# Performance work log

Hardware: AMD Instinct MI355X
Metric: run time of the kernel (lower is better)

The kernel has to match this reference:

```python
import jax, jax.numpy as jnp
import numpy as np
import math

D = 768
H = 12
HD = D // H  # 64
DFF = 4 * D


def _layernorm(x, g, b, eps=1e-5):
    mu = jnp.mean(x, axis=-1, keepdims=True)
    var = jnp.var(x, axis=-1, keepdims=True)
    return (x - mu) * jax.lax.rsqrt(var + eps) * g + b


def _new_gelu(x):
    c = math.sqrt(2.0 / math.pi)
    return 0.5 * x * (1.0 + jnp.tanh(c * (x + 0.044715 * x * x * x)))


def setup_inputs() -> dict:
    key = jax.random.key(0)
    ks = jax.random.split(key, 8)
    B, N = 8, 1024
    s = 0.02
    return {
        "x": jax.random.normal(ks[0], (B, N, D), jnp.float32),
        "pad_mask": jnp.ones((B, N), jnp.int32),
        "ln1_g": jnp.ones((D,), jnp.float32),
        "ln1_b": jnp.zeros((D,), jnp.float32),
        "w_attn": jax.random.normal(ks[1], (D, 3 * D), jnp.float32) * s,
        "b_attn": jnp.zeros((3 * D,), jnp.float32),
        "w_proj": jax.random.normal(ks[2], (D, D), jnp.float32) * s,
        "b_proj": jnp.zeros((D,), jnp.float32),
        "ln2_g": jnp.ones((D,), jnp.float32),
        "ln2_b": jnp.zeros((D,), jnp.float32),
        "w_fc": jax.random.normal(ks[3], (D, DFF), jnp.float32) * s,
        "b_fc": jnp.zeros((DFF,), jnp.float32),
        "w_fc2": jax.random.normal(ks[4], (DFF, D), jnp.float32) * s,
        "b_fc2": jnp.zeros((D,), jnp.float32),
    }


def reference(x, pad_mask, ln1_g, ln1_b, w_attn, b_attn, w_proj, b_proj,
              ln2_g, ln2_b, w_fc, b_fc, w_fc2, b_fc2):
    B, N, C = x.shape
    # --- attention branch (note: source's causal masked_fill is NOT in-place,
    # so the causal mask is effectively never applied; only pad_mask is) ---
    h = _layernorm(x, ln1_g, ln1_b)
    qkv = h @ w_attn + b_attn  # [B,N,3D]
    q, k, v = jnp.split(qkv, 3, axis=-1)
    q = q.reshape(B, N, H, HD).transpose(0, 2, 1, 3)  # [B,H,N,hd]
    k = k.reshape(B, N, H, HD).transpose(0, 2, 1, 3)
    v = v.reshape(B, N, H, HD).transpose(0, 2, 1, 3)
    att = jnp.einsum('bhqd,bhkd->bhqk', q, k) * (1.0 / math.sqrt(HD))
    # pad mask broadcasts as [B,1,N,1]: masks query rows where pad==0
    att = jnp.where(pad_mask[:, None, :, None] == 0, -jnp.inf, att)
    att = jax.nn.softmax(att, axis=-1)
    o = jnp.einsum('bhqk,bhkd->bhqd', att, v)
    o = o.transpose(0, 2, 1, 3).reshape(B, N, C)
    x = x + (o @ w_proj + b_proj)
    # --- MLP branch ---
    h2 = _layernorm(x, ln2_g, ln2_b)
    x = x + (_new_gelu(h2 @ w_fc + b_fc) @ w_fc2 + b_fc2)
    return x
```

## Files before the change

### kernel.cpp

```cpp
#include <hip/hip_runtime.h>
#include <hip/hip_bf16.h>

typedef __bf16 bf16;
typedef __bf16 bf16x8 __attribute__((ext_vector_type(8)));
typedef __bf16 bf16x4 __attribute__((ext_vector_type(4)));
typedef float f32x4 __attribute__((ext_vector_type(4)));

#define SEQ 1024
#define BATCH 8
#define DM 768
#define NH 12
#define HDIM 64
#define DFF 3072
#define NTOK (BATCH*SEQ)

#define AS1 __attribute__((address_space(1)))
#define AS3 __attribute__((address_space(3)))
#define MFMA16(a, b, c) __builtin_amdgcn_mfma_f32_16x16x32_bf16(a, b, c, 0, 0, 0)

__device__ __forceinline__ float gelu_f(float x) {
  const float c = 0.7978845608028654f;
  float z = c * (x + 0.044715f * x * x * x);
  return x / (1.0f + __expf(-2.0f * z));
}

__global__ __launch_bounds__(256) void transpose4_kernel(
    const float* __restrict__ in0, bf16* __restrict__ out0,
    const float* __restrict__ in1, bf16* __restrict__ out1,
    const float* __restrict__ in2, bf16* __restrict__ out2,
    const float* __restrict__ in3, bf16* __restrict__ out3) {
  __shared__ float tile[32][33];
  int id = blockIdx.x;
  const float* in; bf16* out; int R, C;
  if (id < 1728)      { in = in0; out = out0; R = 768;  C = 2304; }
  else if (id < 2304) { in = in1; out = out1; R = 768;  C = 768;  id -= 1728; }
  else if (id < 4608) { in = in2; out = out2; R = 768;  C = 3072; id -= 2304; }
  else                { in = in3; out = out3; R = 3072; C = 768;  id -= 4608; }
  int nc = C >> 5;
  int c0 = (id % nc) * 32, r0 = (id / nc) * 32;
  int tx = threadIdx.x & 31, ty = threadIdx.x >> 5;
  #pragma unroll
  for (int i = 0; i < 4; ++i)
    tile[ty + i * 8][tx] = in[(size_t)(r0 + ty + i * 8) * C + c0 + tx];
  __syncthreads();
  #pragma unroll
  for (int i = 0; i < 4; ++i)
    out[(size_t)(c0 + ty + i * 8) * R + r0 + tx] = (bf16)tile[tx][ty + i * 8];
}

__global__ __launch_bounds__(256) void ln_kernel(
    const float* __restrict__ x, const float* __restrict__ g,
    const float* __restrict__ bta, bf16* __restrict__ out) {
  int row = blockIdx.x;
  int tid = threadIdx.x;
  const float* xr = x + (size_t)row * DM;
  float v0 = xr[tid], v1 = xr[tid + 256], v2 = xr[tid + 512];
  float s1 = v0 + v1 + v2;
  float s2 = v0 * v0 + v1 * v1 + v2 * v2;
  #pragma unroll
  for (int m = 32; m >= 1; m >>= 1) {
    s1 += __shfl_xor(s1, m, 64);
    s2 += __shfl_xor(s2, m, 64);
  }
  __shared__ float ps1[4], ps2[4];
  int wid = tid >> 6;
  if ((tid & 63) == 0) { ps1[wid] = s1; ps2[wid] = s2; }
  __syncthreads();
  float t1 = ps1[0] + ps1[1] + ps1[2] + ps1[3];
  float t2 = ps2[0] + ps2[1] + ps2[2] + ps2[3];
  float mean = t1 * (1.0f / DM);
  float var = t2 * (1.0f / DM) - mean * mean;
  float rstd = rsqrtf(var + 1e-5f);
  bf16* orow = out + (size_t)row * DM;
  orow[tid]       = (bf16)((v0 - mean) * rstd * g[tid]       + bta[tid]);
  orow[tid + 256] = (bf16)((v1 - mean) * rstd * g[tid + 256] + bta[tid + 256]);
  orow[tid + 512] = (bf16)((v2 - mean) * rstd * g[tid + 512] + bta[tid + 512]);
}

__global__ __launch_bounds__(256) void reduce_ln_kernel(
    const float* __restrict__ p0, const float* __restrict__ p1,
    const float* __restrict__ bias, const float* __restrict__ resid,
    const float* __restrict__ g, const float* __restrict__ bta,
    bf16* __restrict__ x1b, bf16* __restrict__ h) {
  int row = blockIdx.x;
  int tid = threadIdx.x;
  size_t base = (size_t)row * DM;
  float v0 = p0[base + tid]       + p1[base + tid]       + bias[tid]       + resid[base + tid];
  float v1 = p0[base + tid + 256] + p1[base + tid + 256] + bias[tid + 256] + resid[base + tid + 256];
  float v2 = p0[base + tid + 512] + p1[base + tid + 512] + bias[tid + 512] + resid[base + tid + 512];
  bf16* xr = x1b + base;
  xr[tid]       = (bf16)v0;
  xr[tid + 256] = (bf16)v1;
  xr[tid + 512] = (bf16)v2;
  float s1 = v0 + v1 + v2;
  float s2 = v0 * v0 + v1 * v1 + v2 * v2;
  #pragma unroll
  for (int m = 32; m >= 1; m >>= 1) {
    s1 += __shfl_xor(s1, m, 64);
    s2 += __shfl_xor(s2, m, 64);
  }
  __shared__ float ps1[4], ps2[4];
  int wid = tid >> 6;
  if ((tid & 63) == 0) { ps1[wid] = s1; ps2[wid] = s2; }
  __syncthreads();
  float t1 = ps1[0] + ps1[1] + ps1[2] + ps1[3];
  float t2 = ps2[0] + ps2[1] + ps2[2] + ps2[3];
  float mean = t1 * (1.0f / DM);
  float var = t2 * (1.0f / DM) - mean * mean;
  float rstd = rsqrtf(var + 1e-5f);
  bf16* orow = h + base;
  orow[tid]       = (bf16)((v0 - mean) * rstd * g[tid]       + bta[tid]);
  orow[tid + 256] = (bf16)((v1 - mean) * rstd * g[tid + 256] + bta[tid + 256]);
  orow[tid + 512] = (bf16)((v2 - mean) * rstd * g[tid + 512] + bta[tid + 512]);
}

__global__ __launch_bounds__(256) void reduce_out_kernel(
    const float* __restrict__ p0, const float* __restrict__ p1,
    const float* __restrict__ bias, const bf16* __restrict__ resid,
    float* __restrict__ out) {
  int i = blockIdx.x * 256 + threadIdx.x;
  size_t e = (size_t)i * 4;
  f32x4 a = *(const f32x4*)(p0 + e);
  f32x4 b = *(const f32x4*)(p1 + e);
  f32x4 bs = *(const f32x4*)(bias + (int)(e % DM));
  bf16x4 r = *(const bf16x4*)(resid + e);
  f32x4 o;
  #pragma unroll
  for (int j = 0; j < 4; ++j) o[j] = a[j] + b[j] + bs[j] + (float)r[j];
  *(f32x4*)(out + e) = o;
}

__global__ __launch_bounds__(512, 4) void gemm_kernel(
    const bf16* __restrict__ A, int lda, const bf16* __restrict__ BT,
    const float* __restrict__ bias, const float* __restrict__ residF,
    const bf16* __restrict__ residB,
    float* __restrict__ outF, bf16* __restrict__ outB,
    int N, int K, int flags) {
  __shared__ bf16 As[3][128 * 32];
  __shared__ bf16 Bs[3][256 * 32];
  int tid = threadIdx.x;
  int wid = tid >> 6, lane = tid & 63;
  int nct = N >> 8;
  int nwg = gridDim.x;
  int bid = blockIdx.x;
  int lid = ((nwg & 7) == 0) ? ((bid & 7) * (nwg >> 3) + (bid >> 3)) : bid;
  int row0, col0, koff = 0, Keff = K;
  size_t outOff = 0;
  if (flags & 2) {
    int half = nwg >> 1;
    int s = lid / half;
    int r = lid - s * half;
    int nrt = half / nct;
    col0 = (r / nrt) << 8;
    row0 = (r % nrt) << 7;
    Keff = K >> 1;
    koff = s * Keff;
    outOff = (size_t)s * ((size_t)nrt << 7) * (size_t)N;
  } else {
    row0 = (lid / nct) * 128;
    col0 = (lid % nct) * 256;
  }
  int wm = wid >> 2, wn = wid & 3;
  int fr = lane & 15, fq = lane >> 4;
  f32x4 acc[4][4] = {};

  int srow = tid >> 2;
  int ssl = ((tid & 3) ^ ((tid >> 3) & 3)) * 8;
  const bf16* gA  = A + (size_t)(row0 + srow) * lda + koff + ssl;
  const bf16* gB  = BT + (size_t)(col0 + srow) * K + koff + ssl;
  const bf16* gB2 = gB + (size_t)128 * K;
  int ldsA  = (wid * 16) * 32;
  int ldsB  = (wid * 16) * 32;
  int ldsB2 = (128 + wid * 16) * 32;

  int RB0 = wn * 64 + 0 * 16 + fr, RB1 = wn * 64 + 1 * 16 + fr;
  int RB2 = wn * 64 + 2 * 16 + fr, RB3 = wn * 64 + 3 * 16 + fr;
  int RA0 = wm * 64 + 0 * 16 + fr, RA1 = wm * 64 + 1 * 16 + fr;
  int RA2 = wm * 64 + 2 * 16 + fr, RA3 = wm * 64 + 3 * 16 + fr;
  int offB0 = RB0 * 32 + (fq ^ ((RB0 >> 1) & 3)) * 8;
  int offB1 = RB1 * 32 + (fq ^ ((RB1 >> 1) & 3)) * 8;
  int offB2 = RB2 * 32 + (fq ^ ((RB2 >> 1) & 3)) * 8;
  int offB3 = RB3 * 32 + (fq ^ ((RB3 >> 1) & 3)) * 8;
  int offA0 = RA0 * 32 + (fq ^ ((RA0 >> 1) & 3)) * 8;
  int offA1 = RA1 * 32 + (fq ^ ((RA1 >> 1) & 3)) * 8;
  int offA2 = RA2 * 32 + (fq ^ ((RA2 >> 1) & 3)) * 8;
  int offA3 = RA3 * 32 + (fq ^ ((RA3 >> 1) & 3)) * 8;

  int nt = Keff >> 5;

  __builtin_amdgcn_global_load_lds((const AS1 void*)(gA), (AS3 void*)(&As[0][ldsA]), 16, 0, 0);
  __builtin_amdgcn_global_load_lds((const AS1 void*)(gB), (AS3 void*)(&Bs[0][ldsB]), 16, 0, 0);
  __builtin_amdgcn_global_load_lds((const AS1 void*)(gB2), (AS3 void*)(&Bs[0][ldsB2]), 16, 0, 0);
  __builtin_amdgcn_global_load_lds((const AS1 void*)(gA + 32), (AS3 void*)(&As[1][ldsA]), 16, 0, 0);
  __builtin_amdgcn_global_load_lds((const AS1 void*)(gB + 32), (AS3 void*)(&Bs[1][ldsB]), 16, 0, 0);
  __builtin_amdgcn_global_load_lds((const AS1 void*)(gB2 + 32), (AS3 void*)(&Bs[1][ldsB2]), 16, 0, 0);

#define KS(CB, T)                                                              \
  {                                                                            \
    if ((T) == nt - 1) asm volatile("s_waitcnt vmcnt(0)" ::: "memory");        \
    else               asm volatile("s_waitcnt vmcnt(3)" ::: "memory");        \
    __builtin_amdgcn_s_barrier();                                              \
    bf16x8 b0 = *(const bf16x8*)&Bs[CB][offB0];                                \
    bf16x8 b1 = *(const bf16x8*)&Bs[CB][offB1];                                \
    bf16x8 b2 = *(const bf16x8*)&Bs[CB][offB2];                                \
    bf16x8 b3 = *(const bf16x8*)&Bs[CB][offB3];                                \
    bf16x8 a0 = *(const bf16x8*)&As[CB][offA0];                                \
    bf16x8 a1 = *(const bf16x8*)&As[CB][offA1];                                \
    if ((T) + 2 < nt)                                                          \
      __builtin_amdgcn_global_load_lds(                                        \
          (const AS1 void*)(gA + ((T) + 2) * 32),                              \
          (AS3 void*)(&As[((CB) + 2) % 3][ldsA]), 16, 0, 0);                   \
    __builtin_amdgcn_s_setprio(1);                                             \
    acc[0][0] = MFMA16(a0, b0, acc[0][0]); acc[0][1] = MFMA16(a0, b1, acc[0][1]); \
    acc[0][2] = MFMA16(a0, b2, acc[0][2]); acc[0][3] = MFMA16(a0, b3, acc[0][3]); \
    acc[1][0] = MFMA16(a1, b0, acc[1][0]); acc[1][1] = MFMA16(a1, b1, acc[1][1]); \
    acc[1][2] = MFMA16(a1, b2, acc[1][2]); acc[1][3] = MFMA16(a1, b3, acc[1][3]); \
    __builtin_amdgcn_s_setprio(0);                                             \
    bf16x8 a2 = *(const bf16x8*)&As[CB][offA2];                                \
    bf16x8 a3 = *(const bf16x8*)&As[CB][offA3];                                \
    if ((T) + 2 < nt) {                                                        \
      __builtin_amdgcn_global_load_lds(                                        \
          (const AS1 void*)(gB + ((T) + 2) * 32),                              \
          (AS3 void*)(&Bs[((CB) + 2) % 3][ldsB]), 16, 0, 0);                   \
      __builtin_amdgcn_global_load_lds(                                        \
          (const AS1 void*)(gB2 + ((T) + 2) * 32),                             \
          (AS3 void*)(&Bs[((CB) + 2) % 3][ldsB2]), 16, 0, 0);                  \
    }                                                                          \
    __builtin_amdgcn_s_setprio(1);                                             \
    acc[2][0] = MFMA16(a2, b0, acc[2][0]); acc[2][1] = MFMA16(a2, b1, acc[2][1]); \
    acc[2][2] = MFMA16(a2, b2, acc[2][2]); acc[2][3] = MFMA16(a2, b3, acc[2][3]); \
    acc[3][0] = MFMA16(a3, b0, acc[3][0]); acc[3][1] = MFMA16(a3, b1, acc[3][1]); \
    acc[3][2] = MFMA16(a3, b2, acc[3][2]); acc[3][3] = MFMA16(a3, b3, acc[3][3]); \
    __builtin_amdgcn_s_setprio(0);                                             \
  }

  for (int t = 0; t < nt; t += 3) {
    KS(0, t);
    KS(1, t + 1);
    KS(2, t + 2);
  }
#undef KS

  bool gelu = (flags & 1);
  bool qkvm = (flags & 4);
  bf16* vtp = (bf16*)outF;
  #pragma unroll
  for (int m = 0; m < 4; ++m) {
    #pragma unroll
    for (int n = 0; n < 4; ++n) {
      int col = col0 + wn * 64 + n * 16 + fr;
      float bs = bias ? bias[col] : 0.f;
      if (qkvm && col >= 2 * DM) {
        int rb = row0 + wm * 64 + m * 16 + fq * 4;
        int hcol = col - 2 * DM;
        int bh = (rb >> 10) * NH + (hcol >> 6);
        bf16x4 vv;
        #pragma unroll
        for (int r = 0; r < 4; ++r) vv[r] = (bf16)(acc[m][n][r] + bs);
        *(bf16x4*)(vtp + ((size_t)bh * HDIM + (hcol & 63)) * SEQ + (rb & 1023)) = vv;
      } else {
        #pragma unroll
        for (int r = 0; r < 4; ++r) {
          int row = row0 + wm * 64 + m * 16 + fq * 4 + r;
          float v = acc[m][n][r] + bs;
          if (gelu) v = gelu_f(v);
          if (residF) v += residF[(size_t)row * N + col];
          if (residB) v += (float)residB[(size_t)row * N + col];
          if (qkvm)        outB[(size_t)row * N + col] = (bf16)v;
          else if (outF)   outF[outOff + (size_t)row * N + col] = v;
          else             outB[(size_t)row * N + col] = (bf16)v;
        }
      }
    }
  }
}

__global__ __launch_bounds__(256) void attn_kernel(
    bf16* __restrict__ qkv, const bf16* __restrict__ vt,
    const int* __restrict__ pad) {
  __shared__ bf16 Ks[2][64 * 64];
  __shared__ bf16 Vs[2][64 * 64];
  __shared__ bf16 P_lds[4][16 * 72];
  int blk = blockIdx.x;
  int lblk = (blk & 7) * 192 + (blk >> 3);
  int qt = lblk & 15;
  int bh = lblk >> 4;
  int b = bh / NH, h = bh % NH;
  int tid = threadIdx.x, wid = tid >> 6, lane = tid & 63;
  int q0 = qt * 64 + wid * 16;
  int fr = lane & 15;
  int fq = lane >> 4;
  int fk = fq * 8;
  const bf16* qbase = qkv + (size_t)(b * SEQ + q0) * (3 * DM) + h * HDIM;
  bf16* Pw = &P_lds[wid][0];
  bf16x8 qf[2];
  #pragma unroll
  for (int kk = 0; kk < 2; ++kk)
    qf[kk] = *(const bf16x8*)(qbase + (size_t)fr * (3 * DM) + kk * 32 + fk);
  int srow = (wid << 4) + (lane >> 3);
  int sc = ((lane & 7) << 4) ^ ((lane >> 3) << 4);
  const bf16* kSrc = qkv + (size_t)(b * SEQ + srow) * (3 * DM) + DM + h * HDIM + (sc >> 1);
  const bf16* vSrc = vt + ((size_t)bh * HDIM + srow) * SEQ + (sc >> 1);

  auto STAGE = [&](int buf, int kt) {
    const bf16* kS = kSrc + (size_t)kt * 64 * (3 * DM);
    const bf16* vS = vSrc + kt * 64;
    bf16* kD = &Ks[buf][wid * 1024];
    bf16* vD = &Vs[buf][wid * 1024];
    __builtin_amdgcn_global_load_lds((const AS1 void*)kS, (AS3 void*)kD, 16, 0, 0);
    __builtin_amdgcn_global_load_lds((const AS1 void*)(kS + 8 * (3 * DM)), (AS3 void*)(kD + 512), 16, 0, 0);
    __builtin_amdgcn_global_load_lds((const AS1 void*)vS, (AS3 void*)vD, 16, 0, 0);
    __builtin_amdgcn_global_load_lds((const AS1 void*)(vS + 8 * SEQ), (AS3 void*)(vD + 512), 16, 0, 0);
  };

  float lp[4] = {0.f, 0.f, 0.f, 0.f};
  f32x4 oacc[4] = {};
  int padv[4];
  #pragma unroll
  for (int r = 0; r < 4; ++r) padv[r] = pad[b * SEQ + q0 + fq * 4 + r];
  bool anymask = __any(padv[0] == 0 || padv[1] == 0 || padv[2] == 0 || padv[3] == 0);
  int xr = (fr & 7) << 4;

  STAGE(0, 0);
  for (int kt = 0; kt < 16; ++kt) {
    int cur = kt & 1;
    if (kt < 15) STAGE(cur ^ 1, kt + 1);
    if (kt == 15) asm volatile("s_waitcnt vmcnt(0)" ::: "memory");
    else          asm volatile("s_waitcnt vmcnt(4)" ::: "memory");
    __builtin_amdgcn_s_barrier();

    f32x4 s[4];
    #pragma unroll
    for (int nt = 0; nt < 4; ++nt) {
      f32x4 a = {};
      #pragma unroll
      for (int kk = 0; kk < 2; ++kk) {
        int colb = (kk * 64 + fq * 16) ^ xr;
        bf16x8 kf = *(const bf16x8*)&Ks[cur][(nt * 16 + fr) * 64 + (colb >> 1)];
        a = __builtin_amdgcn_mfma_f32_16x16x32_bf16(qf[kk], kf, a, 0, 0, 0);
      }
      s[nt] = a;
    }
    if (anymask) {
      #pragma unroll
      for (int r = 0; r < 4; ++r)
        if (padv[r] == 0) { s[0][r] = 0.f; s[1][r] = 0.f; s[2][r] = 0.f; s[3][r] = 0.f; }
    }
    #pragma unroll
    for (int nt = 0; nt < 4; ++nt)
      #pragma unroll
      for (int r = 0; r < 4; ++r)
        s[nt][r] = __expf(s[nt][r] * 0.125f);
    #pragma unroll
    for (int r = 0; r < 4; ++r)
      lp[r] += (s[0][r] + s[1][r]) + (s[2][r] + s[3][r]);
    #pragma unroll
    for (int nt = 0; nt < 4; ++nt)
      #pragma unroll
      for (int r = 0; r < 4; ++r)
        Pw[(fq * 4 + r) * 72 + nt * 16 + fr] = (bf16)s[nt][r];
    #pragma unroll
    for (int nt = 0; nt < 4; ++nt) {
      #pragma unroll
      for (int ks = 0; ks < 2; ++ks) {
        bf16x8 pf = *(const bf16x8*)&Pw[fr * 72 + ks * 32 + fk];
        int colb = (ks * 64 + fq * 16) ^ xr;
        bf16x8 vf = *(const bf16x8*)&Vs[cur][(nt * 16 + fr) * 64 + (colb >> 1)];
        oacc[nt] = __builtin_amdgcn_mfma_f32_16x16x32_bf16(pf, vf, oacc[nt], 0, 0, 0);
      }
    }
    __builtin_amdgcn_s_barrier();
  }
  #pragma unroll
  for (int r = 0; r < 4; ++r) {
    float l = lp[r];
    #pragma unroll
    for (int msk = 8; msk >= 1; msk >>= 1) l += __shfl_xor(l, msk, 64);
    float inv = 1.0f / l;
    #pragma unroll
    for (int nt = 0; nt < 4; ++nt)
      qkv[(size_t)(b * SEQ + q0 + fq * 4 + r) * (3 * DM) + h * HDIM + nt * 16 + fr] =
          (bf16)(oacc[nt][r] * inv);
  }
}

extern "C" void kernel_launch(void* const* d_in, const int* in_sizes, int n_in,
                              void* d_out, int out_size, void* d_ws, size_t ws_size,
                              hipStream_t stream) {
  const float* x      = (const float*)d_in[0];
  const int*   pad    = (const int*)d_in[1];
  const float* ln1_g  = (const float*)d_in[2];
  const float* ln1_b  = (const float*)d_in[3];
  const float* w_attn = (const float*)d_in[4];
  const float* b_attn = (const float*)d_in[5];
  const float* w_proj = (const float*)d_in[6];
  const float* b_proj = (const float*)d_in[7];
  const float* ln2_g  = (const float*)d_in[8];
  const float* ln2_b  = (const float*)d_in[9];
  const float* w_fc   = (const float*)d_in[10];
  const float* b_fc   = (const float*)d_in[11];
  const float* w_fc2  = (const float*)d_in[12];
  const float* b_fc2  = (const float*)d_in[13];
  float* out = (float*)d_out;

  char* ws = (char*)d_ws;
  size_t off = 0;
  auto alloc = [&](size_t bytes) {
    void* p = ws + off;
    off += (bytes + 255) & ~(size_t)255;
    return p;
  };
  bf16* wT_attn = (bf16*)alloc((size_t)(3 * DM) * DM * 2);
  bf16* wT_proj = (bf16*)alloc((size_t)DM * DM * 2);
  bf16* wT_fc   = (bf16*)alloc((size_t)DFF * DM * 2);
  bf16* wT_fc2  = (bf16*)alloc((size_t)DM * DFF * 2);
  bf16* h       = (bf16*)alloc((size_t)NTOK * DM * 2);
  bf16* qkv     = (bf16*)alloc((size_t)NTOK * (3 * DM) * 2);
  bf16* vt      = (bf16*)alloc((size_t)BATCH * NH * HDIM * SEQ * 2);
  bf16* x1b     = (bf16*)alloc((size_t)NTOK * DM * 2);
  bf16* act     = (bf16*)alloc((size_t)NTOK * DFF * 2);

  float* partP = (float*)act;
  float* partF = (float*)h;

  transpose4_kernel<<<6912, 256, 0, stream>>>(
      w_attn, wT_attn, w_proj, wT_proj, w_fc, wT_fc, w_fc2, wT_fc2);
  ln_kernel<<<NTOK, 256, 0, stream>>>(x, ln1_g, ln1_b, h);
  gemm_kernel<<<576, 512, 0, stream>>>(
      h, DM, wT_attn, b_attn, nullptr, nullptr, (float*)vt, qkv, 3 * DM, DM, 4);
  attn_kernel<<<BATCH * NH * (SEQ / 64), 256, 0, stream>>>(qkv, vt, pad);
  gemm_kernel<<<384, 512, 0, stream>>>(
      qkv, 3 * DM, wT_proj, nullptr, nullptr, nullptr, partP, nullptr, DM, DM, 2);
  reduce_ln_kernel<<<NTOK, 256, 0, stream>>>(
      partP, partP + (size_t)NTOK * DM, b_proj, x, ln2_g, ln2_b, x1b, h);
  gemm_kernel<<<768, 512, 0, stream>>>(
      h, DM, wT_fc, b_fc, nullptr, nullptr, nullptr, act, DFF, DM, 1);
  gemm_kernel<<<384, 512, 0, stream>>>(
      act, DFF, wT_fc2, nullptr, nullptr, nullptr, partF, nullptr, DM, DFF, 2);
  reduce_out_kernel<<<(NTOK * DM) / (4 * 256), 256, 0, stream>>>(
      partF, partF + (size_t)NTOK * DM, b_fc2, x1b, out);
}
```

Before: 295.4 us.

## Add 256x256-tile GEMM kernel with 4-stage LDS pipeline for MLP GEMMs

Adds a new GEMM kernel using 256x256 output tiles (8x4 MFMA fragments per wave), four LDS buffers with three loads in flight, and split-K for the second MLP GEMM. The two MLP GEMMs (fc and fc2) switch to it with half the workgroups. Larger tiles raise arithmetic intensity and cut global/LDS traffic per FLOP. The cost is more registers and LDS per block (occupancy 2), fewer blocks (192 for fc2, below the CU count), and tail imbalance.

```diff
diff --git a/kernel.cpp b/kernel.cpp
--- a/kernel.cpp
+++ b/kernel.cpp
@@ -128,6 +128,139 @@
   #pragma unroll
   for (int j = 0; j < 4; ++j) o[j] = a[j] + b[j] + bs[j] + (float)r[j];
   *(f32x4*)(out + e) = o;
+}
+
+__global__ __launch_bounds__(512, 2) void gemm256_kernel(
+    const bf16* __restrict__ A, int lda, const bf16* __restrict__ BT,
+    const float* __restrict__ bias,
+    float* __restrict__ outF, bf16* __restrict__ outB,
+    int N, int K, int flags) {
+  __shared__ bf16 As[4][256 * 32];
+  __shared__ bf16 Bs[4][256 * 32];
+  int tid = threadIdx.x;
+  int wid = tid >> 6, lane = tid & 63;
+  int nct = N >> 8;
+  int nwg = gridDim.x;
+  int bid = blockIdx.x;
+  int lid = (bid & 7) * (nwg >> 3) + (bid >> 3);
+  int row0, col0, koff = 0, Keff = K;
+  size_t outOff = 0;
+  if (flags & 2) {
+    int half = nwg >> 1;
+    int s = lid / half;
+    int r = lid - s * half;
+    int nrt = half / nct;
+    col0 = (r / nrt) << 8;
+    row0 = (r % nrt) << 8;
+    Keff = K >> 1;
+    koff = s * Keff;
+    outOff = (size_t)s * ((size_t)nrt << 8) * (size_t)N;
+  } else {
+    int nrt = nwg / nct;
+    col0 = (lid / nrt) << 8;
+    row0 = (lid % nrt) << 8;
+  }
+  int wm = wid >> 2, wn = wid & 3;
+  int fr = lane & 15, fq = lane >> 4;
+  f32x4 acc[8][4] = {};
+
+  int srow = tid >> 2;
+  int ssl = ((tid & 3) ^ ((tid >> 3) & 3)) * 8;
+  const bf16* gA  = A + (size_t)(row0 + srow) * lda + koff + ssl;
+  const bf16* gA2 = gA + (size_t)128 * lda;
+  const bf16* gB  = BT + (size_t)(col0 + srow) * K + koff + ssl;
+  const bf16* gB2 = gB + (size_t)128 * K;
+  int ldsLo = (wid * 16) * 32;
+  int ldsHi = (128 + wid * 16) * 32;
+
+  int offA[8], offB[4];
+  #pragma unroll
+  for (int m = 0; m < 8; ++m) {
+    int R = wm * 128 + m * 16 + fr;
+    offA[m] = R * 32 + (fq ^ ((R >> 1) & 3)) * 8;
+  }
+  #pragma unroll
+  for (int n = 0; n < 4; ++n) {
+    int R = wn * 64 + n * 16 + fr;
+    offB[n] = R * 32 + (fq ^ ((R >> 1) & 3)) * 8;
+  }
+
+  int nt = Keff >> 5;
+
+  #pragma unroll
+  for (int p = 0; p < 3; ++p) {
+    __builtin_amdgcn_global_load_lds((const AS1 void*)(gA  + p * 32), (AS3 void*)(&As[p][ldsLo]), 16, 0, 0);
+    __builtin_amdgcn_global_load_lds((const AS1 void*)(gA2 + p * 32), (AS3 void*)(&As[p][ldsHi]), 16, 0, 0);
+    __builtin_amdgcn_global_load_lds((const AS1 void*)(gB  + p * 32), (AS3 void*)(&Bs[p][ldsLo]), 16, 0, 0);
+    __builtin_amdgcn_global_load_lds((const AS1 void*)(gB2 + p * 32), (AS3 void*)(&Bs[p][ldsHi]), 16, 0, 0);
+  }
+
+#define KS(CB, T)                                                              \
+  {                                                                            \
+    if ((T) >= nt - 2) {                                                       \
+      if ((T) == nt - 1) asm volatile("s_waitcnt vmcnt(0)" ::: "memory");      \
+      else               asm volatile("s_waitcnt vmcnt(4)" ::: "memory");      \
+    } else               asm volatile("s_waitcnt vmcnt(8)" ::: "memory");      \
+    __builtin_amdgcn_s_barrier();                                              \
+    bf16x8 bb[4], aa[4];                                                       \
+    _Pragma("unroll")                                                          \
+    for (int n = 0; n < 4; ++n) bb[n] = *(const bf16x8*)&Bs[CB][offB[n]];      \
+    _Pragma("unroll")                                                          \
+    for (int m = 0; m < 4; ++m) aa[m] = *(const bf16x8*)&As[CB][offA[m]];      \
+    if ((T) + 3 < nt) {                                                        \
+      __builtin_amdgcn_global_load_lds((const AS1 void*)(gA  + ((T) + 3) * 32),\
+          (AS3 void*)(&As[((CB) + 3) & 3][ldsLo]), 16, 0, 0);                  \
+      __builtin_amdgcn_global_load_lds((const AS1 void*)(gA2 + ((T) + 3) * 32),\
+          (AS3 void*)(&As[((CB) + 3) & 3][ldsHi]), 16, 0, 0);                  \
+      __builtin_amdgcn_global_load_lds((const AS1 void*)(gB  + ((T) + 3) * 32),\
+          (AS3 void*)(&Bs[((CB) + 3) & 3][ldsLo]), 16, 0, 0);                  \
+      __builtin_amdgcn_global_load_lds((const AS1 void*)(gB2 + ((T) + 3) * 32),\
+          (AS3 void*)(&Bs[((CB) + 3) & 3][ldsHi]), 16, 0, 0);                  \
+    }                                                                          \
+    __builtin_amdgcn_s_setprio(1);                                             \
+    _Pragma("unroll")                                                          \
+    for (int m = 0; m < 4; ++m)                                                \
+      _Pragma("unroll")                                                        \
+      for (int n = 0; n < 4; ++n)                                              \
+        acc[m][n] = MFMA16(aa[m], bb[n], acc[m][n]);                           \
+    __builtin_amdgcn_s_setprio(0);                                             \
+    bf16x8 a2[4];                                                              \
+    _Pragma("unroll")                                                          \
+    for (int m = 0; m < 4; ++m) a2[m] = *(const bf16x8*)&As[CB][offA[4 + m]];  \
+    __builtin_amdgcn_s_setprio(1);                                             \
+    _Pragma("unroll")                                                          \
+    for (int m = 0; m < 4; ++m)                                                \
+      _Pragma("unroll")                                                        \
+      for (int n = 0; n < 4; ++n)                                              \
+        acc[4 + m][n] = MFMA16(a2[m], bb[n], acc[4 + m][n]);                   \
+    __builtin_amdgcn_s_setprio(0);                                             \
+  }
+
+  for (int t = 0; t < nt; t += 4) {
+    KS(0, t);
+    KS(1, t + 1);
+    KS(2, t + 2);
+    KS(3, t + 3);
+  }
+#undef KS
+
+  bool gelu = (flags & 1);
+  #pragma unroll
+  for (int m = 0; m < 8; ++m) {
+    #pragma unroll
+    for (int n = 0; n < 4; ++n) {
+      int col = col0 + wn * 64 + n * 16 + fr;
+      float bs = bias ? bias[col] : 0.f;
+      #pragma unroll
+      for (int r = 0; r < 4; ++r) {
+        int row = row0 + wm * 128 + m * 16 + fq * 4 + r;
+        float v = acc[m][n][r] + bs;
+        if (gelu) v = gelu_f(v);
+        if (outF) outF[outOff + (size_t)row * N + col] = v;
+        else outB[(size_t)row * N + col] = (bf16)v;
+      }
+    }
+  }
 }
 
 __global__ __launch_bounds__(512, 4) void gemm_kernel(
@@ -433,10 +566,10 @@
       qkv, 3 * DM, wT_proj, nullptr, nullptr, nullptr, partP, nullptr, DM, DM, 2);
   reduce_ln_kernel<<<NTOK, 256, 0, stream>>>(
       partP, partP + (size_t)NTOK * DM, b_proj, x, ln2_g, ln2_b, x1b, h);
-  gemm_kernel<<<768, 512, 0, stream>>>(
-      h, DM, wT_fc, b_fc, nullptr, nullptr, nullptr, act, DFF, DM, 1);
-  gemm_kernel<<<384, 512, 0, stream>>>(
-      act, DFF, wT_fc2, nullptr, nullptr, nullptr, partF, nullptr, DM, DFF, 2);
+  gemm256_kernel<<<384, 512, 0, stream>>>(
+      h, DM, wT_fc, b_fc, nullptr, act, DFF, DM, 1);
+  gemm256_kernel<<<192, 512, 0, stream>>>(
+      act, DFF, wT_fc2, nullptr, partF, nullptr, DM, DFF, 2);
   reduce_out_kernel<<<(NTOK * DM) / (4 * 256), 256, 0, stream>>>(
       partF, partF + (size_t)NTOK * DM, b_fc2, x1b, out);
 }
```

Result: slower. 301.6 us (+2.1%).
